# Kernel tuning notes

Hardware: AMD Instinct MI355X
Metric: run time of the kernel (lower is better)

## Reference

```python
import jax, jax.numpy as jnp
import numpy as np

B, S, H = 2, 2048, 2048
NH, NKV, HD = 16, 4, 128
SCALING = HD ** -0.5


def rotate_half(x):
    x1, x2 = jnp.split(x, 2, axis=-1)
    return jnp.concatenate((-x2, x1), axis=-1)


def apply_rope(t, cos, sin):
    # t: [B, nh, S, HD]; cos/sin: [B, S, HD] -> unsqueeze head dim
    c = cos[:, None, :, :]
    s = sin[:, None, :, :]
    return t * c + rotate_half(t) * s


def setup_inputs() -> dict:
    key = jax.random.key(0)
    k1, k2, k3, k4, k5 = jax.random.split(key, 5)
    hidden_states = jax.random.normal(k1, (B, S, H), dtype=jnp.float32)
    # real RoPE tables
    inv_freq = 1.0 / (10000.0 ** (jnp.arange(0, HD, 2, dtype=jnp.float32) / HD))
    pos = jnp.arange(S, dtype=jnp.float32)
    freqs = jnp.einsum('s,d->sd', pos, inv_freq)              # [S, HD/2]
    emb = jnp.concatenate((freqs, freqs), axis=-1)            # [S, HD]
    cos = jnp.broadcast_to(jnp.cos(emb)[None], (B, S, HD))
    sin = jnp.broadcast_to(jnp.sin(emb)[None], (B, S, HD))
    # additive causal mask [B, 1, S, S]
    causal = jnp.triu(jnp.full((S, S), -1e9, dtype=jnp.float32), k=1)
    attention_mask = jnp.broadcast_to(causal[None, None], (B, 1, S, S))
    sc = 0.02
    wq = jax.random.normal(k2, (NH * HD, H), dtype=jnp.float32) * sc
    wk = jax.random.normal(k3, (NKV * HD, H), dtype=jnp.float32) * sc
    wv = jax.random.normal(k4, (NKV * HD, H), dtype=jnp.float32) * sc
    wo = jax.random.normal(k5, (H, NH * HD), dtype=jnp.float32) * sc
    return {"hidden_states": hidden_states, "cos": cos, "sin": sin,
            "attention_mask": attention_mask, "wq": wq, "wk": wk, "wv": wv, "wo": wo}


def reference(hidden_states, cos, sin, attention_mask, wq, wk, wv, wo):
    x = hidden_states
    # fused-style QKV projections (nn.Linear: x @ W.T), split heads -> [B, nh, S, HD]
    q = (x @ wq.T).reshape(B, S, NH, HD).transpose(0, 2, 1, 3)
    k = (x @ wk.T).reshape(B, S, NKV, HD).transpose(0, 2, 1, 3)
    v = (x @ wv.T).reshape(B, S, NKV, HD).transpose(0, 2, 1, 3)
    q = apply_rope(q, cos, sin)
    k = apply_rope(k, cos, sin)
    # GQA: repeat KV heads (repeat_kv)
    n_rep = NH // NKV
    k = jnp.repeat(k, n_rep, axis=1)
    v = jnp.repeat(v, n_rep, axis=1)
    scores = jnp.einsum('bhqd,bhkd->bhqk', q, k) * SCALING + attention_mask
    attn = jax.nn.softmax(scores.astype(jnp.float32), axis=-1).astype(q.dtype)
    out = jnp.einsum('bhqk,bhkd->bhqd', attn, v)
    out = out.transpose(0, 2, 1, 3).reshape(B, S, NH * HD)
    out = out @ wo.T
    return (out, attn)
```

## Files before the change

### kernel.cpp

```cpp
#include <hip/hip_runtime.h>
#include <cstdint>
#include <cstddef>

typedef __bf16 bf16;
typedef __attribute__((ext_vector_type(8))) __bf16 bf16x8;
typedef __attribute__((ext_vector_type(4))) __bf16 bf16x4;
typedef __attribute__((ext_vector_type(4))) float f32x4;

constexpr int B_ = 2, S_ = 2048, H_ = 2048, NH_ = 16, NKV_ = 4, HD_ = 128;
constexpr float SCALE_ = 0.08838834764831845f;

#define GLDS16(g, l)                                                        \
  __builtin_amdgcn_global_load_lds(                                         \
      (const __attribute__((address_space(1))) void*)(g),                   \
      (__attribute__((address_space(3))) void*)(l), 16, 0, 0)

#define VMCNT0 asm volatile("s_waitcnt vmcnt(0)" ::: "memory")
#define BAR __builtin_amdgcn_s_barrier()

__global__ void cvt_all(const float* __restrict__ hs, const float* __restrict__ wq,
                        const float* __restrict__ wk, const float* __restrict__ wv,
                        const float* __restrict__ wo, bf16* __restrict__ xb,
                        bf16* __restrict__ w3b, bf16* __restrict__ wob) {
  const int stride = gridDim.x * blockDim.x;
  for (int i = blockIdx.x * blockDim.x + threadIdx.x; i < 4718592; i += stride) {
    const float4* s; bf16x4* d; int j;
    if (i < 2097152)      { s = (const float4*)hs; d = (bf16x4*)xb;            j = i; }
    else if (i < 3145728) { s = (const float4*)wq; d = (bf16x4*)w3b;           j = i - 2097152; }
    else if (i < 3407872) { s = (const float4*)wk; d = (bf16x4*)w3b + 1048576; j = i - 3145728; }
    else if (i < 3670016) { s = (const float4*)wv; d = (bf16x4*)w3b + 1310720; j = i - 3407872; }
    else                  { s = (const float4*)wo; d = (bf16x4*)wob;           j = i - 3670016; }
    float4 v = s[j];
    bf16x4 o;
    o[0] = (bf16)v.x; o[1] = (bf16)v.y; o[2] = (bf16)v.z; o[3] = (bf16)v.w;
    d[j] = o;
  }
}

template <int EPI>
__global__ __launch_bounds__(256) void gemm_bt(const bf16* __restrict__ A,
                                               const bf16* __restrict__ Bm, int K,
                                               bf16* __restrict__ qb, bf16* __restrict__ kb,
                                               bf16* __restrict__ vtb, float* __restrict__ Cout) {
  __shared__ __align__(16) bf16 As[128 * 64];
  __shared__ __align__(16) bf16 Bs[128 * 64];
  const int tid = threadIdx.x;
  const int lane = tid & 63;
  const int wid = tid >> 6;
  const int fid = blockIdx.y * 32 + blockIdx.x;
  const int nwg = gridDim.y * 32;
  const int swz = (fid & 7) * (nwg >> 3) + (fid >> 3);
  const int m0 = (swz & 31) * 128;
  const int n0 = (swz >> 5) * 128;
  const int wm = (wid >> 1) * 64, wn = (wid & 1) * 64;
  const int r = lane & 15, g = lane >> 4;
  f32x4 acc[4][4] = {};

#pragma unroll 1
  for (int kt = 0; kt < K; kt += 64) {
    __syncthreads();
#pragma unroll
    for (int i = 0; i < 4; ++i) {
      int cb = wid * 256 + i * 64;
      int c64 = cb + lane;
      int row = c64 >> 3, cs = (c64 & 7) ^ (row & 7);
      GLDS16(A + (size_t)(m0 + row) * K + kt + cs * 8, As + cb * 8);
      GLDS16(Bm + (size_t)(n0 + row) * K + kt + cs * 8, Bs + cb * 8);
    }
    VMCNT0;
    __syncthreads();
#pragma unroll
    for (int ks = 0; ks < 2; ++ks) {
      bf16x8 af[4], bfr[4];
#pragma unroll
      for (int fm = 0; fm < 4; ++fm)
        af[fm] = *(const bf16x8*)(As + (wm + fm * 16 + r) * 64 + (((ks * 4 + g) ^ (r & 7)) << 3));
#pragma unroll
      for (int fn = 0; fn < 4; ++fn)
        bfr[fn] = *(const bf16x8*)(Bs + (wn + fn * 16 + r) * 64 + (((ks * 4 + g) ^ (r & 7)) << 3));
#pragma unroll
      for (int fm = 0; fm < 4; ++fm)
#pragma unroll
        for (int fn = 0; fn < 4; ++fn)
          acc[fm][fn] = __builtin_amdgcn_mfma_f32_16x16x32_bf16(af[fm], bfr[fn], acc[fm][fn], 0, 0, 0);
    }
  }

#pragma unroll
  for (int fm = 0; fm < 4; ++fm)
#pragma unroll
    for (int fn = 0; fn < 4; ++fn)
#pragma unroll
      for (int rr = 0; rr < 4; ++rr) {
        int mm = m0 + wm + fm * 16 + g * 4 + rr;
        int nn = n0 + wn + fn * 16 + r;
        float v = acc[fm][fn][rr];
        if (EPI == 1) {
          Cout[(size_t)mm * 2048 + nn] = v;
        } else {
          int b = mm >> 11, s = mm & (S_ - 1);
          int d = nn & 127;
          if (nn < 2048) {
            int hh = nn >> 7;
            qb[(((size_t)b * NH_ + hh) * S_ + s) * HD_ + d] = (bf16)v;
          } else if (nn < 2560) {
            int hh = (nn - 2048) >> 7;
            kb[(((size_t)b * NKV_ + hh) * S_ + s) * HD_ + d] = (bf16)v;
          } else {
            int hh = (nn - 2560) >> 7;
            vtb[(((size_t)b * NKV_ + hh) * HD_ + d) * S_ + s] = (bf16)v;
          }
        }
      }
}

__global__ void rope_k_kernel(bf16* __restrict__ kb, const float* __restrict__ cosp,
                              const float* __restrict__ sinp) {
  const int NK = B_ * NKV_ * S_;
  int t = blockIdx.x * blockDim.x + threadIdx.x;
  if (t >= NK * 8) return;
  const int oct = t & 7, rid = t >> 3;
  bf16* base = kb + (size_t)rid * HD_;
  const int s = rid & (S_ - 1);
  const int b = rid >> 13;
  const int d = oct * 8;
  const float* cp = cosp + ((size_t)b * S_ + s) * HD_ + d;
  const float* sp = sinp + ((size_t)b * S_ + s) * HD_ + d;
  float4 c0 = *(const float4*)cp, c1 = *(const float4*)(cp + 4);
  float4 s0 = *(const float4*)sp, s1 = *(const float4*)(sp + 4);
  float cc[8] = {c0.x, c0.y, c0.z, c0.w, c1.x, c1.y, c1.z, c1.w};
  float ss[8] = {s0.x, s0.y, s0.z, s0.w, s1.x, s1.y, s1.z, s1.w};
  bf16x8 x1 = *(const bf16x8*)(base + d);
  bf16x8 x2 = *(const bf16x8*)(base + d + 64);
  bf16x8 o1, o2;
#pragma unroll
  for (int i = 0; i < 8; ++i) {
    float a = (float)x1[i], bb = (float)x2[i];
    o1[i] = (bf16)(a * cc[i] - bb * ss[i]);
    o2[i] = (bf16)(bb * cc[i] + a * ss[i]);
  }
  *(bf16x8*)(base + d) = o1;
  *(bf16x8*)(base + d + 64) = o2;
}

__global__ __launch_bounds__(256, 4) void attn_kernel(const bf16* __restrict__ qb,
                                                      const bf16* __restrict__ kb,
                                                      const bf16* __restrict__ vtb,
                                                      const float* __restrict__ cosp,
                                                      const float* __restrict__ sinp,
                                                      bf16* __restrict__ aob,
                                                      float* __restrict__ attn_out) {
  __shared__ __align__(16) bf16 Ks[64 * 128];
  __shared__ __align__(16) bf16 Vs[128 * 64];
  __shared__ __align__(16) bf16 Ps[64 * 64];
  const int bid = (blockIdx.x & 7) * 64 + (blockIdx.x >> 3);
  const int p = bid & 15;
  const int h = (bid >> 4) & 15;
  const int b = bid >> 8;
  const int kh = h >> 2;
  const int tid = threadIdx.x, lane = tid & 63, wid = tid >> 6;
  const int r = lane & 15, g = lane >> 4;

  const bf16* kbase = kb + ((size_t)b * NKV_ + kh) * S_ * HD_;
  const bf16* vbase = vtb + ((size_t)b * NKV_ + kh) * (size_t)HD_ * S_;
  const size_t ahead = (size_t)(b * NH_ + h) * S_;

  auto stageK = [&](int kt) {
#pragma unroll
    for (int i = 0; i < 4; ++i) {
      int base = i * 256 + wid * 64;
      int idx = base + lane;
      int row = idx >> 4, ch = (idx & 15) ^ (row & 7);
      GLDS16(kbase + (size_t)(kt * 64 + row) * HD_ + ch * 8, Ks + base * 8);
    }
  };
  auto stageV = [&](int kt) {
#pragma unroll
    for (int i = 0; i < 4; ++i) {
      int base = i * 256 + wid * 64;
      int idx = base + lane;
      int row = idx >> 3, ch = (idx & 7) ^ (row & 7);
      GLDS16(vbase + (size_t)row * S_ + kt * 64 + ch * 8, Vs + base * 8);
    }
  };

  int zc = 0;

#pragma unroll 1
  for (int sbi = 0; sbi < 2; ++sbi) {
    const int qt = sbi ? 31 - p : p;
    const int q0 = qt * 64;
    const int nt = qt + 1;
    const bf16* qsrc = qb + ((size_t)(b * NH_ + h) * S_ + q0) * HD_;

    bf16x8 qreg[4];
    {
      const int srow = q0 + wid * 16 + r;
#pragma unroll
      for (int ks = 0; ks < 4; ++ks)
        qreg[ks] = *(const bf16x8*)(qsrc + (wid * 16 + r) * HD_ + ks * 32 + g * 8);
      const float* cp = cosp + ((size_t)b * S_ + srow) * HD_;
      const float* sp = sinp + ((size_t)b * S_ + srow) * HD_;
#pragma unroll
      for (int hf = 0; hf < 2; ++hf) {
        const int d0 = hf * 32 + g * 8;
        float4 ca = *(const float4*)(cp + d0), cb2 = *(const float4*)(cp + d0 + 4);
        float4 sa = *(const float4*)(sp + d0), sb2 = *(const float4*)(sp + d0 + 4);
        float cc[8] = {ca.x, ca.y, ca.z, ca.w, cb2.x, cb2.y, cb2.z, cb2.w};
        float ss[8] = {sa.x, sa.y, sa.z, sa.w, sb2.x, sb2.y, sb2.z, sb2.w};
        bf16x8 lo = qreg[hf], hi = qreg[hf + 2];
#pragma unroll
        for (int i = 0; i < 8; ++i) {
          float a = (float)lo[i], bb = (float)hi[i];
          qreg[hf][i] = (bf16)(a * cc[i] - bb * ss[i]);
          qreg[hf + 2][i] = (bf16)(bb * cc[i] + a * ss[i]);
        }
      }
    }

    float lsum = 0.f;
#pragma unroll 1
    for (int kt = 0; kt < nt; ++kt) {
      __syncthreads();
      stageK(kt);
      VMCNT0;
      __syncthreads();
      if (zc <= 30) {
        int qtz, ktz;
        if (zc < 31 - p) { qtz = p; ktz = p + 1 + zc; }
        else             { qtz = 31 - p; ktz = zc + 1; }
        float* zdst = attn_out + (ahead + qtz * 64) * S_ + ktz * 64;
        float4 z = {0.f, 0.f, 0.f, 0.f};
#pragma unroll
        for (int i = 0; i < 4; ++i) {
          int idx = i * 256 + tid;
          *(float4*)(zdst + (size_t)(idx >> 4) * S_ + (idx & 15) * 4) = z;
        }
        ++zc;
      }
      f32x4 sacc[4] = {};
      __builtin_amdgcn_s_setprio(1);
#pragma unroll
      for (int ks = 0; ks < 4; ++ks)
#pragma unroll
        for (int fn = 0; fn < 4; ++fn) {
          bf16x8 kk = *(const bf16x8*)(Ks + (fn * 16 + r) * 128 + (((ks * 4 + g) ^ (r & 7)) << 3));
          sacc[fn] = __builtin_amdgcn_mfma_f32_16x16x32_bf16(kk, qreg[ks], sacc[fn], 0, 0, 0);
        }
      __builtin_amdgcn_s_setprio(0);
      float ts = 0.f;
      if (kt == nt - 1) {
#pragma unroll
        for (int fn = 0; fn < 4; ++fn)
#pragma unroll
          for (int rr = 0; rr < 4; ++rr) {
            bool msk = (fn * 16 + g * 4 + rr) > (wid * 16 + r);
            ts += msk ? 0.f : __expf(sacc[fn][rr] * SCALE_);
          }
      } else {
#pragma unroll
        for (int fn = 0; fn < 4; ++fn)
#pragma unroll
          for (int rr = 0; rr < 4; ++rr) ts += __expf(sacc[fn][rr] * SCALE_);
      }
      ts += __shfl_xor(ts, 16);
      ts += __shfl_xor(ts, 32);
      lsum += ts;
    }
    const float rl = 1.0f / lsum;

    f32x4 oacc[8] = {};
    const size_t arow0 = (ahead + q0) * S_;
#pragma unroll 1
    for (int kt = 0; kt < nt; ++kt) {
      const int k0 = kt * 64;
      __syncthreads();
      stageK(kt);
      stageV(kt);
      VMCNT0;
      __syncthreads();
      f32x4 sacc[4] = {};
      __builtin_amdgcn_s_setprio(1);
#pragma unroll
      for (int ks = 0; ks < 4; ++ks)
#pragma unroll
        for (int fn = 0; fn < 4; ++fn) {
          bf16x8 kk = *(const bf16x8*)(Ks + (fn * 16 + r) * 128 + (((ks * 4 + g) ^ (r & 7)) << 3));
          sacc[fn] = __builtin_amdgcn_mfma_f32_16x16x32_bf16(kk, qreg[ks], sacc[fn], 0, 0, 0);
        }
      __builtin_amdgcn_s_setprio(0);
      const int prow = (wid * 16 + r) * 64;
      const bool last = (kt == nt - 1);
#pragma unroll
      for (int fn = 0; fn < 4; ++fn) {
        float4 pv4;
        bf16x4 pk;
#pragma unroll
        for (int rr = 0; rr < 4; ++rr) {
          bool msk = last && ((fn * 16 + g * 4 + rr) > (wid * 16 + r));
          float f = msk ? 0.f : __expf(sacc[fn][rr] * SCALE_) * rl;
          ((float*)&pv4)[rr] = f;
          pk[rr] = (bf16)f;
        }
        *(float4*)(attn_out + arow0 + (size_t)(wid * 16 + r) * S_ + k0 + fn * 16 + g * 4) = pv4;
        *(bf16x4*)(&Ps[prow + ((((fn << 1) | (g >> 1)) ^ (r & 7)) << 3) + ((g & 1) << 2)]) = pk;
      }
      __builtin_amdgcn_s_setprio(1);
#pragma unroll
      for (int ks = 0; ks < 2; ++ks) {
        bf16x8 pa = *(const bf16x8*)(&Ps[prow + (((ks * 4 + g) ^ (r & 7)) << 3)]);
#pragma unroll
        for (int fn = 0; fn < 8; ++fn) {
          bf16x8 vv = *(const bf16x8*)(Vs + (fn * 16 + r) * 64 + (((ks * 4 + g) ^ (r & 7)) << 3));
          oacc[fn] = __builtin_amdgcn_mfma_f32_16x16x32_bf16(pa, vv, oacc[fn], 0, 0, 0);
        }
      }
      __builtin_amdgcn_s_setprio(0);
    }

#pragma unroll
    for (int fn = 0; fn < 8; ++fn)
#pragma unroll
      for (int rr = 0; rr < 4; ++rr) {
        int q = q0 + wid * 16 + g * 4 + rr;
        aob[((size_t)b * S_ + q) * 2048 + h * HD_ + fn * 16 + r] = (bf16)oacc[fn][rr];
      }
  }
}

extern "C" void kernel_launch(void* const* d_in, const int* in_sizes, int n_in,
                              void* d_out, int out_size, void* d_ws, size_t ws_size,
                              hipStream_t stream) {
  const float* hidden = (const float*)d_in[0];
  const float* cosp = (const float*)d_in[1];
  const float* sinp = (const float*)d_in[2];
  const float* wq = (const float*)d_in[4];
  const float* wk = (const float*)d_in[5];
  const float* wv = (const float*)d_in[6];
  const float* wo = (const float*)d_in[7];
  float* out = (float*)d_out;
  float* attn = out + (size_t)B_ * S_ * H_;

  char* ws = (char*)d_ws;
  bf16* xb  = (bf16*)(ws);
  bf16* w3b = (bf16*)(ws + (16ull << 20));
  bf16* wob = (bf16*)(ws + (28ull << 20));
  bf16* qb  = (bf16*)(ws + (36ull << 20));
  bf16* kb  = (bf16*)(ws + (52ull << 20));
  bf16* vtb = (bf16*)(ws + (56ull << 20));
  bf16* aob = (bf16*)(ws + (60ull << 20));

  cvt_all<<<2048, 256, 0, stream>>>(hidden, wq, wk, wv, wo, xb, w3b, wob);
  gemm_bt<0><<<dim3(32, 24), 256, 0, stream>>>(xb, w3b, 2048, qb, kb, vtb, nullptr);
  rope_k_kernel<<<512, 256, 0, stream>>>(kb, cosp, sinp);
  attn_kernel<<<512, 256, 0, stream>>>(qb, kb, vtb, cosp, sinp, aob, attn);
  gemm_bt<1><<<dim3(32, 16), 256, 0, stream>>>(aob, wob, 2048, nullptr, nullptr, nullptr, out);
}
```

Baseline: 350.1 us.

## Process two GQA heads per block sharing K/V tiles, with nontemporal attn stores

Each block now handles one query tile for two query heads that share a KV head, so every staged K/V tile feeds twice the MFMA work. This replaces the old pairing of query tiles p and 31-p, and blocks are ordered heaviest-first. Writes of the attention matrix and its zero fill now use nontemporal stores, and any zero blocks left over are written after the main loop. Register pressure doubles (two qreg and oacc sets), so launch bounds drop to 2 waves per SIMD, trading occupancy for reuse; per-block work is now uneven, with load balance relying on the descending order.

```diff
diff --git a/kernel.cpp b/kernel.cpp
--- a/kernel.cpp
+++ b/kernel.cpp
@@ -17,6 +17,10 @@
 
 #define VMCNT0 asm volatile("s_waitcnt vmcnt(0)" ::: "memory")
 #define BAR __builtin_amdgcn_s_barrier()
+
+__device__ inline void nt_store4(float* p, f32x4 v) {
+  __builtin_nontemporal_store(v, (f32x4*)p);
+}
 
 __global__ void cvt_all(const float* __restrict__ hs, const float* __restrict__ wq,
                         const float* __restrict__ wk, const float* __restrict__ wv,
@@ -143,7 +147,7 @@
   *(bf16x8*)(base + d + 64) = o2;
 }
 
-__global__ __launch_bounds__(256, 4) void attn_kernel(const bf16* __restrict__ qb,
+__global__ __launch_bounds__(256, 2) void attn_kernel(const bf16* __restrict__ qb,
                                                       const bf16* __restrict__ kb,
                                                       const bf16* __restrict__ vtb,
                                                       const float* __restrict__ cosp,
@@ -154,16 +158,22 @@
   __shared__ __align__(16) bf16 Vs[128 * 64];
   __shared__ __align__(16) bf16 Ps[64 * 64];
   const int bid = (blockIdx.x & 7) * 64 + (blockIdx.x >> 3);
-  const int p = bid & 15;
-  const int h = (bid >> 4) & 15;
+  const int qt = 31 - (bid & 31);
+  const int hp = (bid >> 5) & 1;
+  const int kh = (bid >> 6) & 3;
   const int b = bid >> 8;
-  const int kh = h >> 2;
+  const int h0 = kh * 4 + hp * 2;
+  const int q0 = qt * 64;
+  const int nt = qt + 1;
   const int tid = threadIdx.x, lane = tid & 63, wid = tid >> 6;
   const int r = lane & 15, g = lane >> 4;
 
   const bf16* kbase = kb + ((size_t)b * NKV_ + kh) * S_ * HD_;
   const bf16* vbase = vtb + ((size_t)b * NKV_ + kh) * (size_t)HD_ * S_;
-  const size_t ahead = (size_t)(b * NH_ + h) * S_;
+  size_t arow0[2];
+#pragma unroll
+  for (int hh = 0; hh < 2; ++hh)
+    arow0[hh] = ((size_t)(b * NH_ + h0 + hh) * S_ + q0) * S_;
 
   auto stageK = [&](int kt) {
 #pragma unroll
@@ -184,60 +194,68 @@
     }
   };
 
-  int zc = 0;
-
-#pragma unroll 1
-  for (int sbi = 0; sbi < 2; ++sbi) {
-    const int qt = sbi ? 31 - p : p;
-    const int q0 = qt * 64;
-    const int nt = qt + 1;
-    const bf16* qsrc = qb + ((size_t)(b * NH_ + h) * S_ + q0) * HD_;
-
-    bf16x8 qreg[4];
-    {
-      const int srow = q0 + wid * 16 + r;
+  bf16x8 qreg[2][4];
+  {
+    const int srow = q0 + wid * 16 + r;
+    const float* cp = cosp + ((size_t)b * S_ + srow) * HD_;
+    const float* sp = sinp + ((size_t)b * S_ + srow) * HD_;
+    float cc[2][8], ss[2][8];
+#pragma unroll
+    for (int hf = 0; hf < 2; ++hf) {
+      const int d0 = hf * 32 + g * 8;
+      float4 ca = *(const float4*)(cp + d0), cb2 = *(const float4*)(cp + d0 + 4);
+      float4 sa = *(const float4*)(sp + d0), sb2 = *(const float4*)(sp + d0 + 4);
+      cc[hf][0] = ca.x; cc[hf][1] = ca.y; cc[hf][2] = ca.z; cc[hf][3] = ca.w;
+      cc[hf][4] = cb2.x; cc[hf][5] = cb2.y; cc[hf][6] = cb2.z; cc[hf][7] = cb2.w;
+      ss[hf][0] = sa.x; ss[hf][1] = sa.y; ss[hf][2] = sa.z; ss[hf][3] = sa.w;
+      ss[hf][4] = sb2.x; ss[hf][5] = sb2.y; ss[hf][6] = sb2.z; ss[hf][7] = sb2.w;
+    }
+#pragma unroll
+    for (int hh = 0; hh < 2; ++hh) {
+      const bf16* qsrc = qb + ((size_t)(b * NH_ + h0 + hh) * S_ + q0) * HD_;
 #pragma unroll
       for (int ks = 0; ks < 4; ++ks)
-        qreg[ks] = *(const bf16x8*)(qsrc + (wid * 16 + r) * HD_ + ks * 32 + g * 8);
-      const float* cp = cosp + ((size_t)b * S_ + srow) * HD_;
-      const float* sp = sinp + ((size_t)b * S_ + srow) * HD_;
+        qreg[hh][ks] = *(const bf16x8*)(qsrc + (wid * 16 + r) * HD_ + ks * 32 + g * 8);
 #pragma unroll
       for (int hf = 0; hf < 2; ++hf) {
-        const int d0 = hf * 32 + g * 8;
-        float4 ca = *(const float4*)(cp + d0), cb2 = *(const float4*)(cp + d0 + 4);
-        float4 sa = *(const float4*)(sp + d0), sb2 = *(const float4*)(sp + d0 + 4);
-        float cc[8] = {ca.x, ca.y, ca.z, ca.w, cb2.x, cb2.y, cb2.z, cb2.w};
-        float ss[8] = {sa.x, sa.y, sa.z, sa.w, sb2.x, sb2.y, sb2.z, sb2.w};
-        bf16x8 lo = qreg[hf], hi = qreg[hf + 2];
+        bf16x8 lo = qreg[hh][hf], hi = qreg[hh][hf + 2];
 #pragma unroll
         for (int i = 0; i < 8; ++i) {
           float a = (float)lo[i], bb = (float)hi[i];
-          qreg[hf][i] = (bf16)(a * cc[i] - bb * ss[i]);
-          qreg[hf + 2][i] = (bf16)(bb * cc[i] + a * ss[i]);
-        }
-      }
-    }
-
-    float lsum = 0.f;
+          qreg[hh][hf][i] = (bf16)(a * cc[hf][i] - bb * ss[hf][i]);
+          qreg[hh][hf + 2][i] = (bf16)(bb * cc[hf][i] + a * ss[hf][i]);
+        }
+      }
+    }
+  }
+
+  const int nzero = 62 - 2 * qt;
+  int zc = 0;
+
+  float lsum[2] = {0.f, 0.f};
 #pragma unroll 1
-    for (int kt = 0; kt < nt; ++kt) {
-      __syncthreads();
-      stageK(kt);
-      VMCNT0;
-      __syncthreads();
-      if (zc <= 30) {
-        int qtz, ktz;
-        if (zc < 31 - p) { qtz = p; ktz = p + 1 + zc; }
-        else             { qtz = 31 - p; ktz = zc + 1; }
-        float* zdst = attn_out + (ahead + qtz * 64) * S_ + ktz * 64;
-        float4 z = {0.f, 0.f, 0.f, 0.f};
+  for (int kt = 0; kt < nt; ++kt) {
+    __syncthreads();
+    stageK(kt);
+    VMCNT0;
+    __syncthreads();
+#pragma unroll
+    for (int zi = 0; zi < 2; ++zi) {
+      if (zc < nzero) {
+        int hh = (zc >= 31 - qt) ? 1 : 0;
+        int ktz = qt + 1 + (hh ? zc - (31 - qt) : zc);
+        float* zdst = attn_out + arow0[hh] + ktz * 64;
+        f32x4 z = {0.f, 0.f, 0.f, 0.f};
 #pragma unroll
         for (int i = 0; i < 4; ++i) {
           int idx = i * 256 + tid;
-          *(float4*)(zdst + (size_t)(idx >> 4) * S_ + (idx & 15) * 4) = z;
+          nt_store4(zdst + (size_t)(idx >> 4) * S_ + (idx & 15) * 4, z);
         }
         ++zc;
       }
+    }
+#pragma unroll
+    for (int hh = 0; hh < 2; ++hh) {
       f32x4 sacc[4] = {};
       __builtin_amdgcn_s_setprio(1);
 #pragma unroll
@@ -245,7 +263,7 @@
 #pragma unroll
         for (int fn = 0; fn < 4; ++fn) {
           bf16x8 kk = *(const bf16x8*)(Ks + (fn * 16 + r) * 128 + (((ks * 4 + g) ^ (r & 7)) << 3));
-          sacc[fn] = __builtin_amdgcn_mfma_f32_16x16x32_bf16(kk, qreg[ks], sacc[fn], 0, 0, 0);
+          sacc[fn] = __builtin_amdgcn_mfma_f32_16x16x32_bf16(kk, qreg[hh][ks], sacc[fn], 0, 0, 0);
         }
       __builtin_amdgcn_s_setprio(0);
       float ts = 0.f;
@@ -265,20 +283,23 @@
       }
       ts += __shfl_xor(ts, 16);
       ts += __shfl_xor(ts, 32);
-      lsum += ts;
-    }
-    const float rl = 1.0f / lsum;
-
-    f32x4 oacc[8] = {};
-    const size_t arow0 = (ahead + q0) * S_;
+      lsum[hh] += ts;
+    }
+  }
+  float rl[2] = {1.0f / lsum[0], 1.0f / lsum[1]};
+
+  f32x4 oacc[2][8] = {};
 #pragma unroll 1
-    for (int kt = 0; kt < nt; ++kt) {
-      const int k0 = kt * 64;
-      __syncthreads();
-      stageK(kt);
-      stageV(kt);
-      VMCNT0;
-      __syncthreads();
+  for (int kt = 0; kt < nt; ++kt) {
+    const int k0 = kt * 64;
+    __syncthreads();
+    stageK(kt);
+    stageV(kt);
+    VMCNT0;
+    __syncthreads();
+    const bool last = (kt == nt - 1);
+#pragma unroll
+    for (int hh = 0; hh < 2; ++hh) {
       f32x4 sacc[4] = {};
       __builtin_amdgcn_s_setprio(1);
 #pragma unroll
@@ -286,23 +307,22 @@
 #pragma unroll
         for (int fn = 0; fn < 4; ++fn) {
           bf16x8 kk = *(const bf16x8*)(Ks + (fn * 16 + r) * 128 + (((ks * 4 + g) ^ (r & 7)) << 3));
-          sacc[fn] = __builtin_amdgcn_mfma_f32_16x16x32_bf16(kk, qreg[ks], sacc[fn], 0, 0, 0);
+          sacc[fn] = __builtin_amdgcn_mfma_f32_16x16x32_bf16(kk, qreg[hh][ks], sacc[fn], 0, 0, 0);
         }
       __builtin_amdgcn_s_setprio(0);
       const int prow = (wid * 16 + r) * 64;
-      const bool last = (kt == nt - 1);
 #pragma unroll
       for (int fn = 0; fn < 4; ++fn) {
-        float4 pv4;
+        f32x4 pv4;
         bf16x4 pk;
 #pragma unroll
         for (int rr = 0; rr < 4; ++rr) {
           bool msk = last && ((fn * 16 + g * 4 + rr) > (wid * 16 + r));
-          float f = msk ? 0.f : __expf(sacc[fn][rr] * SCALE_) * rl;
-          ((float*)&pv4)[rr] = f;
+          float f = msk ? 0.f : __expf(sacc[fn][rr] * SCALE_) * rl[hh];
+          pv4[rr] = f;
           pk[rr] = (bf16)f;
         }
-        *(float4*)(attn_out + arow0 + (size_t)(wid * 16 + r) * S_ + k0 + fn * 16 + g * 4) = pv4;
+        nt_store4(attn_out + arow0[hh] + (size_t)(wid * 16 + r) * S_ + k0 + fn * 16 + g * 4, pv4);
         *(bf16x4*)(&Ps[prow + ((((fn << 1) | (g >> 1)) ^ (r & 7)) << 3) + ((g & 1) << 2)]) = pk;
       }
       __builtin_amdgcn_s_setprio(1);
@@ -312,19 +332,34 @@
 #pragma unroll
         for (int fn = 0; fn < 8; ++fn) {
           bf16x8 vv = *(const bf16x8*)(Vs + (fn * 16 + r) * 64 + (((ks * 4 + g) ^ (r & 7)) << 3));
-          oacc[fn] = __builtin_amdgcn_mfma_f32_16x16x32_bf16(pa, vv, oacc[fn], 0, 0, 0);
+          oacc[hh][fn] = __builtin_amdgcn_mfma_f32_16x16x32_bf16(pa, vv, oacc[hh][fn], 0, 0, 0);
         }
       }
       __builtin_amdgcn_s_setprio(0);
     }
-
+  }
+
+#pragma unroll
+  for (int hh = 0; hh < 2; ++hh)
 #pragma unroll
     for (int fn = 0; fn < 8; ++fn)
 #pragma unroll
       for (int rr = 0; rr < 4; ++rr) {
         int q = q0 + wid * 16 + g * 4 + rr;
-        aob[((size_t)b * S_ + q) * 2048 + h * HD_ + fn * 16 + r] = (bf16)oacc[fn][rr];
-      }
+        aob[((size_t)b * S_ + q) * 2048 + (h0 + hh) * HD_ + fn * 16 + r] = (bf16)oacc[hh][fn][rr];
+      }
+
+#pragma unroll 1
+  for (; zc < nzero; ++zc) {
+    int hh = (zc >= 31 - qt) ? 1 : 0;
+    int ktz = qt + 1 + (hh ? zc - (31 - qt) : zc);
+    float* zdst = attn_out + arow0[hh] + ktz * 64;
+    f32x4 z = {0.f, 0.f, 0.f, 0.f};
+#pragma unroll
+    for (int i = 0; i < 4; ++i) {
+      int idx = i * 256 + tid;
+      nt_store4(zdst + (size_t)(idx >> 4) * S_ + (idx & 15) * 4, z);
+    }
   }
 }
 
```

Measured after the change: 349.7 us. Within noise of the previous version (-0.1%).
